# Optimization experiments

Hardware: AMD Instinct MI355X
Metric: run time of the kernel (lower is better)

The kernel has to match this reference:

```python
import jax, jax.numpy as jnp
import numpy as np

B, R, C, A, K = 32, 13, 13, 5, 20
CELL = K + 5                      # 4 coords + objectness + 20 classes
N = R * C * A                     # 845 boxes per image
THRESH = 0.5
NMS_TH = 0.4
BIAS_VALS = [1.3221, 1.73145, 3.19275, 4.00944, 5.05587,
             8.09892, 9.47112, 4.84053, 11.2364, 10.0071]


def setup_inputs() -> dict:
    key = jax.random.key(0)
    x = jax.random.normal(key, (B, R, C, A * CELL), dtype=jnp.float32)
    bias = jnp.array(BIAS_VALS, dtype=jnp.float32)  # anchor priors (w,h interleaved)
    return {"x": x, "bias": bias}


def _nms_keep(iou, scores):
    """Greedy per-class NMS. iou: [B,N,N]; scores: [B,K,N] (already thresholded).
    Returns bool keep mask [B,K,N]. Decisions are non-differentiable, so inputs
    are stop_gradient'ed by the caller."""
    Bn = scores.shape[0]
    valid = scores > THRESH
    order = jnp.argsort(-scores, axis=-1)          # descending score order [B,K,N]
    rank = jnp.argsort(order, axis=-1)             # inverse permutation   [B,K,N]
    barange = jnp.arange(Bn)[:, None]

    def body(i, suppressed):
        idx = order[:, :, i]                                              # [B,K]
        sup_i = jnp.take_along_axis(suppressed, idx[:, :, None], -1)[..., 0]
        val_i = jnp.take_along_axis(valid, idx[:, :, None], -1)[..., 0]
        alive = val_i & ~sup_i                                            # [B,K]
        row = iou[barange, idx]                                           # [B,K,N]
        return suppressed | (alive[..., None] & (row > NMS_TH) & (rank > i))

    suppressed = jax.lax.fori_loop(0, N, body, jnp.zeros((Bn, K, N), bool))
    return valid & ~suppressed


def reference(x, bias):
    Bn, R_, C_, _ = x.shape
    t = x.reshape(Bn, R_, C_, A, CELL)
    gx = jnp.arange(C_, dtype=x.dtype)
    gy = jnp.arange(R_, dtype=x.dtype)
    # box decode (matches source: hNorm=rows used for width, wNorm=cols for height)
    bx = (jax.nn.sigmoid(t[..., 0]) + gx[None, None, :, None]) / C_
    by = (jax.nn.sigmoid(t[..., 1]) + gy[None, :, None, None]) / R_
    bw = jnp.exp(t[..., 2]) * bias[0::2] / R_
    bh = jnp.exp(t[..., 3]) * bias[1::2] / C_
    obj = jax.nn.sigmoid(t[..., 4])
    cls = jax.nn.softmax(t[..., 5:], axis=-1)
    prob = obj[..., None] * cls
    prob = jnp.where(prob > THRESH, prob, 0.0)

    # flatten to box index layout (y*cols + x)*anchors + a, same as source
    flat = lambda a: a.reshape(Bn, N)
    bx, by, bw, bh, obj = map(flat, (bx, by, bw, bh, obj))
    prob = prob.reshape(Bn, N, K)

    # corner-form boxes for IoU (source uses x - w/2, y - h/2, w, h)
    x1 = bx - bw * 0.5
    y1 = by - bh * 0.5
    x2 = x1 + bw
    y2 = y1 + bh
    iw = jnp.maximum(0.0, jnp.minimum(x2[:, :, None], x2[:, None, :]) -
                          jnp.maximum(x1[:, :, None], x1[:, None, :]))
    ih = jnp.maximum(0.0, jnp.minimum(y2[:, :, None], y2[:, None, :]) -
                          jnp.maximum(y1[:, :, None], y1[:, None, :]))
    inter = iw * ih
    area = bw * bh
    union = area[:, :, None] + area[:, None, :] - inter
    iou = inter / jnp.maximum(union, 1e-9)                       # [B,N,N]

    scores = prob.transpose(0, 2, 1)                             # [B,K,N]
    keep = _nms_keep(jax.lax.stop_gradient(iou),
                     jax.lax.stop_gradient(scores))
    out_prob = jnp.where(keep, scores, 0.0).transpose(0, 2, 1)   # [B,N,K]

    out = jnp.concatenate([bx[..., None], by[..., None], bw[..., None],
                           bh[..., None], obj[..., None], out_prob], axis=-1)
    return out  # [B, N, CELL]
```

## Files before the change

### kernel.cpp

```cpp
#include <hip/hip_runtime.h>
#include <math.h>

#define BN 32
#define RR 13
#define CC 13
#define AA 5
#define KK 20
#define CELLSZ 25
#define NN (RR * CC * AA)
#define THRESH 0.5f
#define NMS_TH 0.4f

__device__ __forceinline__ float sigmoidf_(float x) {
    return 1.0f / (1.0f + expf(-x));
}

__global__ void decode_kernel(const float* __restrict__ x,
                              const float* __restrict__ bias,
                              float* __restrict__ out) {
    int idx = blockIdx.x * blockDim.x + threadIdx.x;
    if (idx >= BN * NN) return;
    int b = idx / NN;
    int n = idx % NN;
    int r = n / (CC * AA);
    int rem = n % (CC * AA);
    int c = rem / AA;
    int a = rem % AA;

    const float* t = x + (((size_t)(b * RR + r) * CC + c) * AA + a) * CELLSZ;

    float t0 = t[0], t1 = t[1], t2 = t[2], t3 = t[3], t4 = t[4];
    float bx = (sigmoidf_(t0) + (float)c) / (float)CC;
    float by = (sigmoidf_(t1) + (float)r) / (float)RR;
    float bw = expf(t2) * bias[2 * a] / (float)RR;
    float bh = expf(t3) * bias[2 * a + 1] / (float)CC;
    float obj = sigmoidf_(t4);

    float cl[KK];
    float m = t[5];
#pragma unroll
    for (int k = 1; k < KK; ++k) m = fmaxf(m, t[5 + k]);
    float s = 0.0f;
#pragma unroll
    for (int k = 0; k < KK; ++k) { cl[k] = expf(t[5 + k] - m); s += cl[k]; }

    float* o = out + (size_t)(b * NN + n) * CELLSZ;
    o[0] = bx; o[1] = by; o[2] = bw; o[3] = bh; o[4] = obj;
#pragma unroll
    for (int k = 0; k < KK; ++k) {
        float p = obj * (cl[k] / s);
        o[5 + k] = (p > THRESH) ? p : 0.0f;
    }
}

__global__ void nms_kernel(float* __restrict__ out) {
    __shared__ float sx1[NN], sy1[NN], sx2[NN], sy2[NN], sar[NN], ssc[NN];
    __shared__ unsigned char st[NN];
    __shared__ float red_s[256];
    __shared__ int   red_i[256];

    int b = blockIdx.x / KK;
    int k = blockIdx.x % KK;
    int tid = threadIdx.x;

    for (int n = tid; n < NN; n += 256) {
        const float* o = out + (size_t)(b * NN + n) * CELLSZ;
        float bx = o[0], by = o[1], bw = o[2], bh = o[3];
        float x1 = bx - bw * 0.5f;
        float y1 = by - bh * 0.5f;
        sx1[n] = x1;
        sy1[n] = y1;
        sx2[n] = x1 + bw;
        sy2[n] = y1 + bh;
        sar[n] = bw * bh;
        float sc = o[5 + k];
        ssc[n] = sc;
        st[n] = (sc > THRESH) ? 0 : 1;
    }
    __syncthreads();

    while (true) {
        float best = -1.0f;
        int bi = 0x7fffffff;
        for (int n = tid; n < NN; n += 256) {
            if (st[n] == 0) {
                float sc = ssc[n];
                if (sc > best || (sc == best && n < bi)) { best = sc; bi = n; }
            }
        }
        red_s[tid] = best;
        red_i[tid] = bi;
        __syncthreads();
#pragma unroll
        for (int off = 128; off > 0; off >>= 1) {
            if (tid < off) {
                float so = red_s[tid + off];
                int   io = red_i[tid + off];
                if (so > red_s[tid] || (so == red_s[tid] && io < red_i[tid])) {
                    red_s[tid] = so;
                    red_i[tid] = io;
                }
            }
            __syncthreads();
        }
        float bsc = red_s[0];
        int   sel = red_i[0];
        __syncthreads();

        if (bsc < 0.0f) break;

        if (tid == 0) st[sel] = 2;

        float X1 = sx1[sel], Y1 = sy1[sel], X2 = sx2[sel], Y2 = sy2[sel];
        float AR = sar[sel];
        for (int n = tid; n < NN; n += 256) {
            if (n != sel && st[n] == 0) {
                float iw = fmaxf(0.0f, fminf(X2, sx2[n]) - fmaxf(X1, sx1[n]));
                float ih = fmaxf(0.0f, fminf(Y2, sy2[n]) - fmaxf(Y1, sy1[n]));
                float inter = iw * ih;
                float uni = AR + sar[n] - inter;
                float iou = inter / fmaxf(uni, 1e-9f);
                if (iou > NMS_TH) st[n] = 1;
            }
        }
        __syncthreads();
    }

    for (int n = tid; n < NN; n += 256) {
        if (ssc[n] > THRESH && st[n] != 2) {
            out[(size_t)(b * NN + n) * CELLSZ + 5 + k] = 0.0f;
        }
    }
}

extern "C" void kernel_launch(void* const* d_in, const int* in_sizes, int n_in,
                              void* d_out, int out_size, void* d_ws, size_t ws_size,
                              hipStream_t stream) {
    const float* x    = (const float*)d_in[0];
    const float* bias = (const float*)d_in[1];
    float* out = (float*)d_out;

    decode_kernel<<<(BN * NN + 255) / 256, 256, 0, stream>>>(x, bias, out);
    nms_kernel<<<BN * KK, 256, 0, stream>>>(out);
}
```

Measured before the change: 69.66 us.

## Fuse decode into NMS kernel and use wave-shuffle argmax reduction

Merges the decode and NMS kernels into one launch. Each (batch, class) block recomputes box decode and the softmax score for its own class straight from the input, and only class-0 blocks write the box fields. This removes a launch and the round trip of intermediate output through global memory, at the cost of redoing the decode and softmax 20 times per box. The argmax reduction is also changed from a shared-memory tree with a barrier per step to a 64-lane partial fold followed by wavefront shuffles, which cuts the number of barriers per NMS iteration.

```diff
diff --git a/kernel.cpp b/kernel.cpp
--- a/kernel.cpp
+++ b/kernel.cpp
@@ -10,62 +10,46 @@
 #define NN (RR * CC * AA)
 #define THRESH 0.5f
 #define NMS_TH 0.4f
+#define NT 256
 
 __device__ __forceinline__ float sigmoidf_(float x) {
     return 1.0f / (1.0f + expf(-x));
 }
 
-__global__ void decode_kernel(const float* __restrict__ x,
-                              const float* __restrict__ bias,
-                              float* __restrict__ out) {
-    int idx = blockIdx.x * blockDim.x + threadIdx.x;
-    if (idx >= BN * NN) return;
-    int b = idx / NN;
-    int n = idx % NN;
-    int r = n / (CC * AA);
-    int rem = n % (CC * AA);
-    int c = rem / AA;
-    int a = rem % AA;
-
-    const float* t = x + (((size_t)(b * RR + r) * CC + c) * AA + a) * CELLSZ;
-
-    float t0 = t[0], t1 = t[1], t2 = t[2], t3 = t[3], t4 = t[4];
-    float bx = (sigmoidf_(t0) + (float)c) / (float)CC;
-    float by = (sigmoidf_(t1) + (float)r) / (float)RR;
-    float bw = expf(t2) * bias[2 * a] / (float)RR;
-    float bh = expf(t3) * bias[2 * a + 1] / (float)CC;
-    float obj = sigmoidf_(t4);
-
-    float cl[KK];
-    float m = t[5];
-#pragma unroll
-    for (int k = 1; k < KK; ++k) m = fmaxf(m, t[5 + k]);
-    float s = 0.0f;
-#pragma unroll
-    for (int k = 0; k < KK; ++k) { cl[k] = expf(t[5 + k] - m); s += cl[k]; }
-
-    float* o = out + (size_t)(b * NN + n) * CELLSZ;
-    o[0] = bx; o[1] = by; o[2] = bw; o[3] = bh; o[4] = obj;
-#pragma unroll
-    for (int k = 0; k < KK; ++k) {
-        float p = obj * (cl[k] / s);
-        o[5 + k] = (p > THRESH) ? p : 0.0f;
-    }
-}
-
-__global__ void nms_kernel(float* __restrict__ out) {
+__global__ __launch_bounds__(NT) void region_fused_kernel(
+        const float* __restrict__ x,
+        const float* __restrict__ bias,
+        float* __restrict__ out) {
     __shared__ float sx1[NN], sy1[NN], sx2[NN], sy2[NN], sar[NN], ssc[NN];
     __shared__ unsigned char st[NN];
-    __shared__ float red_s[256];
-    __shared__ int   red_i[256];
+    __shared__ float red_s[NT];
+    __shared__ int   red_i[NT];
 
-    int b = blockIdx.x / KK;
-    int k = blockIdx.x % KK;
-    int tid = threadIdx.x;
+    const int b   = blockIdx.x / KK;
+    const int k   = blockIdx.x % KK;
+    const int tid = threadIdx.x;
 
-    for (int n = tid; n < NN; n += 256) {
-        const float* o = out + (size_t)(b * NN + n) * CELLSZ;
-        float bx = o[0], by = o[1], bw = o[2], bh = o[3];
+    for (int n = tid; n < NN; n += NT) {
+        int r   = n / (CC * AA);
+        int rem = n % (CC * AA);
+        int c   = rem / AA;
+        int a   = rem % AA;
+        const float* t = x + (((size_t)(b * RR + r) * CC + c) * AA + a) * CELLSZ;
+
+        float bx  = (sigmoidf_(t[0]) + (float)c) / (float)CC;
+        float by  = (sigmoidf_(t[1]) + (float)r) / (float)RR;
+        float bw  = expf(t[2]) * bias[2 * a]     / (float)RR;
+        float bh  = expf(t[3]) * bias[2 * a + 1] / (float)CC;
+        float obj = sigmoidf_(t[4]);
+
+        float m = t[5];
+#pragma unroll
+        for (int j = 1; j < KK; ++j) m = fmaxf(m, t[5 + j]);
+        float s = 0.0f;
+#pragma unroll
+        for (int j = 0; j < KK; ++j) s += expf(t[5 + j] - m);
+        float sck = obj * (expf(t[5 + k] - m) / s);
+
         float x1 = bx - bw * 0.5f;
         float y1 = by - bh * 0.5f;
         sx1[n] = x1;
@@ -73,39 +57,48 @@
         sx2[n] = x1 + bw;
         sy2[n] = y1 + bh;
         sar[n] = bw * bh;
-        float sc = o[5 + k];
-        ssc[n] = sc;
-        st[n] = (sc > THRESH) ? 0 : 1;
+        ssc[n] = sck;
+        st[n]  = (sck > THRESH) ? 0 : 1;
+
+        if (k == 0) {
+            float* o = out + (size_t)(b * NN + n) * CELLSZ;
+            o[0] = bx; o[1] = by; o[2] = bw; o[3] = bh; o[4] = obj;
+        }
     }
     __syncthreads();
 
     while (true) {
         float best = -1.0f;
-        int bi = 0x7fffffff;
-        for (int n = tid; n < NN; n += 256) {
+        int   bi   = 0x7fffffff;
+        for (int n = tid; n < NN; n += NT) {
             if (st[n] == 0) {
                 float sc = ssc[n];
-                if (sc > best || (sc == best && n < bi)) { best = sc; bi = n; }
+                if (sc > best) { best = sc; bi = n; }
             }
         }
         red_s[tid] = best;
         red_i[tid] = bi;
         __syncthreads();
+        if (tid < 64) {
+            float s0 = red_s[tid];
+            int   i0 = red_i[tid];
 #pragma unroll
-        for (int off = 128; off > 0; off >>= 1) {
-            if (tid < off) {
+            for (int off = 64; off < NT; off += 64) {
                 float so = red_s[tid + off];
                 int   io = red_i[tid + off];
-                if (so > red_s[tid] || (so == red_s[tid] && io < red_i[tid])) {
-                    red_s[tid] = so;
-                    red_i[tid] = io;
-                }
+                if (so > s0 || (so == s0 && io < i0)) { s0 = so; i0 = io; }
             }
-            __syncthreads();
+#pragma unroll
+            for (int off = 32; off > 0; off >>= 1) {
+                float so = __shfl_down(s0, off);
+                int   io = __shfl_down(i0, off);
+                if (so > s0 || (so == s0 && io < i0)) { s0 = so; i0 = io; }
+            }
+            if (tid == 0) { red_s[0] = s0; red_i[0] = i0; }
         }
+        __syncthreads();
         float bsc = red_s[0];
         int   sel = red_i[0];
-        __syncthreads();
 
         if (bsc < 0.0f) break;
 
@@ -113,23 +106,21 @@
 
         float X1 = sx1[sel], Y1 = sy1[sel], X2 = sx2[sel], Y2 = sy2[sel];
         float AR = sar[sel];
-        for (int n = tid; n < NN; n += 256) {
+        for (int n = tid; n < NN; n += NT) {
             if (n != sel && st[n] == 0) {
                 float iw = fmaxf(0.0f, fminf(X2, sx2[n]) - fmaxf(X1, sx1[n]));
                 float ih = fmaxf(0.0f, fminf(Y2, sy2[n]) - fmaxf(Y1, sy1[n]));
                 float inter = iw * ih;
-                float uni = AR + sar[n] - inter;
-                float iou = inter / fmaxf(uni, 1e-9f);
+                float uni   = AR + sar[n] - inter;
+                float iou   = inter / fmaxf(uni, 1e-9f);
                 if (iou > NMS_TH) st[n] = 1;
             }
         }
         __syncthreads();
     }
 
-    for (int n = tid; n < NN; n += 256) {
-        if (ssc[n] > THRESH && st[n] != 2) {
-            out[(size_t)(b * NN + n) * CELLSZ + 5 + k] = 0.0f;
-        }
+    for (int n = tid; n < NN; n += NT) {
+        out[(size_t)(b * NN + n) * CELLSZ + 5 + k] = (st[n] == 2) ? ssc[n] : 0.0f;
     }
 }
 
@@ -140,6 +131,5 @@
     const float* bias = (const float*)d_in[1];
     float* out = (float*)d_out;
 
-    decode_kernel<<<(BN * NN + 255) / 256, 256, 0, stream>>>(x, bias, out);
-    nms_kernel<<<BN * KK, 256, 0, stream>>>(out);
+    region_fused_kernel<<<BN * KK, NT, 0, stream>>>(x, bias, out);
 }
```

Measured after the change: 72.72 us. 4.4% more time.
